# Kernel tuning notes

Measured on AMD Instinct MI355X. Metric: run time of the kernel, lower is better.

The kernel has to match this reference:

```python
import jax, jax.numpy as jnp
import numpy as np

B, S, H = 4, 1024, 2048
E = 16            # num_experts
K = 2             # num_experts_per_token
I = 1024          # per-expert intermediate_dim
N_SHARED = 2
I_SHARED = I * N_SHARED
RATIO = 0.1       # shared_expert_ratio
EPS = 1e-9


def _swiglu(x, wg, wu, wd):
    # SwiGLU, bias=False: down( silu(gate(x)) * up(x) )
    return (jax.nn.silu(x @ wg) * (x @ wu)) @ wd


def setup_inputs() -> dict:
    key = jax.random.key(0)
    ks = jax.random.split(key, 9)
    scale = 0.02
    x = jax.random.normal(ks[0], (B, S, H), dtype=jnp.float32)
    centroids = jax.random.normal(ks[1], (E, H), dtype=jnp.float32)  # nn.Parameter(randn)
    gate_bias = jnp.zeros((E,), dtype=jnp.float32)
    # shared expert SwiGLU weights (intermediate = I * n_shared_experts)
    wg_s = jax.random.normal(ks[2], (H, I_SHARED), dtype=jnp.float32) * scale
    wu_s = jax.random.normal(ks[3], (H, I_SHARED), dtype=jnp.float32) * scale
    wd_s = jax.random.normal(ks[4], (I_SHARED, H), dtype=jnp.float32) * scale
    # routed experts, stacked [E, ...]
    wg = jax.random.normal(ks[5], (E, H, I), dtype=jnp.float32) * scale
    wu = jax.random.normal(ks[6], (E, H, I), dtype=jnp.float32) * scale
    wd = jax.random.normal(ks[7], (E, I, H), dtype=jnp.float32) * scale
    return {"x": x, "centroids": centroids, "gate_bias": gate_bias,
            "wg_s": wg_s, "wu_s": wu_s, "wd_s": wd_s,
            "wg": wg, "wu": wu, "wd": wd}


def reference(x, centroids, gate_bias, wg_s, wu_s, wd_s, wg, wu, wd):
    # 1) shared expert on ALL tokens, scaled by ratio
    shared = _swiglu(x, wg_s, wu_s, wd_s) * RATIO          # [B,S,H]
    # 2) centroid affinity (DeepSeek-V3 sigmoid gating)
    affinity = jax.nn.sigmoid(jnp.einsum('bsh,eh->bse', x, centroids))  # [B,S,E]
    # 3) bias used ONLY for selection
    biased = affinity + gate_bias
    _, top_idx = jax.lax.top_k(biased, K)                  # [B,S,K]
    # 4) clean weights from unbiased affinity, normalized to sum 1
    top_aff = jnp.take_along_axis(affinity, top_idx, axis=-1)  # [B,S,K]
    weights = top_aff / (top_aff.sum(-1, keepdims=True) + EPS)
    # 5) combine-mask: per-token per-expert weight (0 if not selected)
    mask = (jax.nn.one_hot(top_idx, E, dtype=x.dtype) * weights[..., None]).sum(-2)  # [B,S,E]
    # 6) expert compute + weighted combine; loop over fixed small E avoids
    #    materializing a [B,S,E,H] tensor
    routed = jnp.zeros_like(x)
    for e in range(E):
        routed = routed + mask[..., e:e + 1] * _swiglu(x, wg[e], wu[e], wd[e])
    return shared + routed
```

## Files before the change

kernel.cpp:

```cpp
#include <hip/hip_runtime.h>
#include <hip/hip_bf16.h>

typedef unsigned short u16;
typedef unsigned int u32;
typedef unsigned long long u64;
typedef __attribute__((ext_vector_type(8))) short short8;
typedef __attribute__((ext_vector_type(4))) float f32x4;

#define TOKENS 4096
#define HDIM 2048
#define NEXP 16
#define IDIM 1024
#define ISH 2048
#define NCHUNK 128

#define GUITEMS 2304
#define GUCHUNK 288
#define DITEMS 2048
#define DCHUNK 256

#define AS1(p) ((const __attribute__((address_space(1))) u32*)(p))
#define AS3(p) ((__attribute__((address_space(3))) u32*)(p))

__device__ __forceinline__ u16 f2b(float f) {
    u32 u = __float_as_uint(f);
    u32 r = u + 0x7fffu + ((u >> 16) & 1u);
    return (u16)(r >> 16);
}

__global__ __launch_bounds__(256) void convert_x_kernel(const float* __restrict__ x,
                                                        u16* __restrict__ xb) {
    size_t i = ((size_t)blockIdx.x * 256 + threadIdx.x) * 8;
    float4 a = *(const float4*)(x + i);
    float4 b = *(const float4*)(x + i + 4);
    u32 p0 = (u32)f2b(a.x) | ((u32)f2b(a.y) << 16);
    u32 p1 = (u32)f2b(a.z) | ((u32)f2b(a.w) << 16);
    u32 p2 = (u32)f2b(b.x) | ((u32)f2b(b.y) << 16);
    u32 p3 = (u32)f2b(b.z) | ((u32)f2b(b.w) << 16);
    uint4 o = make_uint4(p0, p1, p2, p3);
    *(uint4*)(xb + i) = o;
}

__global__ __launch_bounds__(256) void route_kernel(const float* __restrict__ x,
                                                    const float* __restrict__ cent,
                                                    const float* __restrict__ bias,
                                                    int* __restrict__ top_e,
                                                    float* __restrict__ top_w) {
    __shared__ alignas(16) float cs[8 * 2048];
    int lane = threadIdx.x & 63;
    int wv = threadIdx.x >> 6;
    int t = blockIdx.x * 4 + wv;
    const float4* xp4 = (const float4*)(x + (size_t)t * HDIM);
    float4 xr[8];
#pragma unroll
    for (int i = 0; i < 8; i++) xr[i] = xp4[lane + 64 * i];
    float aff[16];
#pragma unroll
    for (int ph = 0; ph < 2; ph++) {
        if (ph) __syncthreads();
        const float* sbase = cent + (size_t)(ph * 8 + wv * 2) * HDIM;
        float* dbase = cs + (size_t)wv * 2 * HDIM;
#pragma unroll
        for (int i = 0; i < 16; i++) {
            __builtin_amdgcn_global_load_lds(AS1(sbase + i * 256 + lane * 4),
                                             AS3(dbase + i * 256), 16, 0, 0);
        }
        __syncthreads();
#pragma unroll
        for (int e = 0; e < 8; e++) {
            const float4* cp = (const float4*)cs + (size_t)e * 512;
            float s = 0.f;
#pragma unroll
            for (int i = 0; i < 8; i++) {
                float4 cv = cp[lane + 64 * i];
                s += xr[i].x * cv.x;
                s += xr[i].y * cv.y;
                s += xr[i].z * cv.z;
                s += xr[i].w * cv.w;
            }
#pragma unroll
            for (int off = 32; off > 0; off >>= 1) s += __shfl_xor(s, off, 64);
            aff[ph * 8 + e] = 1.f / (1.f + expf(-s));
        }
    }
    float b0 = -1e30f, b1 = -1e30f, a0 = 0.f, a1 = 0.f;
    int e0 = -1, e1 = -1;
#pragma unroll
    for (int e = 0; e < 16; e++) {
        float v = aff[e] + bias[e];
        if (v > b0) {
            b1 = b0; e1 = e0; a1 = a0;
            b0 = v; e0 = e; a0 = aff[e];
        } else if (v > b1) {
            b1 = v; e1 = e; a1 = aff[e];
        }
    }
    float inv = 1.f / (a0 + a1 + 1e-9f);
    if (lane == 0) {
        top_e[2 * t] = e0; top_w[2 * t] = a0 * inv;
        top_e[2 * t + 1] = e1; top_w[2 * t + 1] = a1 * inv;
    }
}

__global__ __launch_bounds__(1024) void build_kernel(
    const int* __restrict__ top_e, const float* __restrict__ top_w,
    int* __restrict__ counts, int* __restrict__ offsets, int* __restrict__ itemsGU,
    int* __restrict__ itemsD, int* __restrict__ list_tok, int* __restrict__ tok2slot) {
    __shared__ int cnt[NCHUNK][16];
    __shared__ int offs_s[16];
    __shared__ int totals[16];
    __shared__ int guPref[16], dPref[16];
    int tid = threadIdx.x;
    int lane = tid & 63, wv = tid >> 6;
    for (int i = tid; i < GUITEMS; i += 1024) itemsGU[i] = -1;
    for (int i = tid; i < DITEMS; i += 1024) itemsD[i] = -1;
    for (int c = wv; c < NCHUNK; c += 16) {
        int v = top_e[c * 64 + lane];
#pragma unroll
        for (int e = 0; e < 16; e++) {
            u64 m = __ballot(v == e);
            if (lane == 0) cnt[c][e] = (int)__popcll(m);
        }
    }
    __syncthreads();
    if (tid < 16) {
        int s = 0;
        for (int c = 0; c < NCHUNK; c++) s += cnt[c][tid];
        totals[tid] = s;
        counts[tid] = s;
    }
    __syncthreads();
    if (tid == 0) {
        int r = 0, g = 0, d = 0;
        for (int e = 0; e < 16; e++) {
            offs_s[e] = r;
            offsets[e] = r;
            r += totals[e];
            guPref[e] = g;
            g += ((totals[e] + 127) >> 7) * 16;
            dPref[e] = d;
            d += ((totals[e] + 255) >> 8) * 32;
        }
    }
    {
        int i = tid;
        int g = i >> 4, s = i & 15;
        int y0 = (g >> 3) << 2, m0 = (g & 7) << 2;
        itemsGU[i] = ((m0 + (s >> 2)) << 8) | (y0 + (s & 3));
    }
    if (tid < 512) {
        int i = tid;
        int g = i >> 4, s = i & 15;
        int y0 = (g >> 2) << 2, m0 = (g & 3) << 2;
        itemsD[i] = ((m0 + (s >> 2)) << 8) | (y0 + (s & 3));
    }
    __syncthreads();
    if (tid < 16) {
        int e = tid;
        int tA = (totals[e] + 127) >> 7;
        int p = 1024 + guPref[e];
        for (int y0 = 0; y0 < 16; y0 += 4)
            for (int m = 0; m < tA; m++)
                for (int dy = 0; dy < 4; dy++)
                    itemsGU[p++] = (1 << 28) | (e << 20) | (m << 8) | (y0 + dy);
        int tB = (totals[e] + 255) >> 8;
        p = 512 + dPref[e];
        for (int y0 = 0; y0 < 32; y0 += 4)
            for (int m = 0; m < tB; m++)
                for (int dy = 0; dy < 4; dy++)
                    itemsD[p++] = (1 << 28) | (e << 20) | (m << 8) | (y0 + dy);
        int r = offs_s[e];
        for (int c = 0; c < NCHUNK; c++) {
            int v = cnt[c][e];
            cnt[c][e] = r;
            r += v;
        }
    }
    __syncthreads();
    for (int c = wv; c < NCHUNK; c += 16) {
        int i = c * 64 + lane;
        int v = top_e[i];
        int rank = 0;
#pragma unroll
        for (int e = 0; e < 16; e++) {
            u64 m = __ballot(v == e);
            if (v == e) rank = (int)__popcll(m & ((1ull << lane) - 1ull));
        }
        int slot = cnt[c][v] + rank;
        list_tok[slot] = i >> 1;
        tok2slot[i] = slot;
    }
}

__global__ __launch_bounds__(256) void conv_w_kernel(const float* __restrict__ W,
                                                     const float* __restrict__ W2,
                                                     u16* __restrict__ Wt,
                                                     u16* __restrict__ Wt2, int K, int N,
                                                     int zsplit) {
    int nt = blockIdx.x, kc = blockIdx.y;
    int zz = blockIdx.z;
    const float* Wm;
    u16* Wtm;
    if (zz < zsplit) {
        Wm = W + (size_t)zz * K * N;
        Wtm = Wt + (size_t)zz * K * N;
    } else {
        int z2 = zz - zsplit;
        Wm = W2 + (size_t)z2 * K * N;
        Wtm = Wt2 + (size_t)z2 * K * N;
    }
    int ksB = K >> 5;
    __shared__ u16 Ls[64 * 40];
    int t = threadIdx.x;
    int kr = t >> 3, ng = t & 7;
    int nn = t >> 2, seg = t & 3;
    int g = seg ^ ((nn >> 2) & 3);
#pragma unroll
    for (int s = 0; s < 8; s++) {
        int kb = kc * 256 + s * 32;
        const float* src = Wm + (size_t)(kb + kr) * N + nt * 64 + ng * 8;
        float4 f0 = *(const float4*)src;
        float4 f1 = *(const float4*)(src + 4);
        __syncthreads();
        const float* p0 = (const float*)&f0;
        const float* p1 = (const float*)&f1;
#pragma unroll
        for (int l = 0; l < 4; l++) Ls[(8 * ng + l) * 40 + kr] = f2b(p0[l]);
#pragma unroll
        for (int l = 0; l < 4; l++) Ls[(8 * ng + 4 + l) * 40 + kr] = f2b(p1[l]);
        __syncthreads();
        const u16* lp = &Ls[nn * 40 + g * 8];
        u32 w0 = (u32)lp[0] | ((u32)lp[1] << 16);
        u32 w1 = (u32)lp[2] | ((u32)lp[3] << 16);
        u32 w2 = (u32)lp[4] | ((u32)lp[5] << 16);
        u32 w3 = (u32)lp[6] | ((u32)lp[7] << 16);
        uint4 o = make_uint4(w0, w1, w2, w3);
        *(uint4*)(Wtm + (size_t)(nt * ksB + (kb >> 5)) * 2048 + t * 8) = o;
    }
}

__global__ __launch_bounds__(256) void gemm_gateup(
    const u16* __restrict__ A, const u16* __restrict__ BgS, const u16* __restrict__ BuS,
    const u16* __restrict__ BgR, const u16* __restrict__ BuR, u16* __restrict__ hS,
    u16* __restrict__ hR, const int* __restrict__ counts, const int* __restrict__ offsets,
    const int* __restrict__ list_tok, const int* __restrict__ items) {
    int idx = (blockIdx.x & 7) * GUCHUNK + (blockIdx.x >> 3);
    int it = items[idx];
    if (it < 0) return;
    int routed = (it >> 28) & 1;
    int e = (it >> 20) & 15;
    int m0 = ((it >> 8) & 4095) * 128;
    int yb = it & 255;
    int cnt, base, Nout;
    const u16 *Bg, *Bu;
    u16* hout;
    if (routed) {
        cnt = counts[e];
        base = offsets[e];
        Nout = IDIM;
        size_t off = (size_t)e * HDIM * IDIM;
        Bg = BgR + off;
        Bu = BuR + off;
        hout = hR;
    } else {
        cnt = TOKENS;
        base = 0;
        Nout = ISH;
        Bg = BgS;
        Bu = BuS;
        hout = hS;
    }
    const int nk = HDIM >> 6;
    __shared__ alignas(16) u16 As[128 * 64];
    __shared__ alignas(16) u16 Bgs[64 * 64];
    __shared__ alignas(16) u16 Bus[64 * 64];
    int tid = threadIdx.x;
    int lane = tid & 63, wv = tid >> 6;
    int quad = lane >> 4, mr = lane & 15;
    int n0 = yb * 64;
    int gk = (tid & 3) ^ ((tid >> 4) & 3);
    int mg0 = min(m0 + (tid >> 2), cnt - 1);
    int mg1 = min(m0 + 64 + (tid >> 2), cnt - 1);
    size_t sr0 = routed ? (size_t)list_tok[base + mg0] : (size_t)mg0;
    size_t sr1 = routed ? (size_t)list_tok[base + mg1] : (size_t)mg1;
    const u16* ap0 = A + sr0 * HDIM + gk * 8;
    const u16* ap1 = A + sr1 * HDIM + gk * 8;
    size_t bstr = (size_t)(HDIM >> 5) * 2048;
    const u16* bgp = Bg + (size_t)yb * bstr + tid * 8;
    const u16* bup = Bu + (size_t)yb * bstr + tid * 8;
    int xq = quad ^ ((mr >> 2) & 3);
    f32x4 accg[2][4], accu[2][4];
#pragma unroll
    for (int i = 0; i < 2; i++)
#pragma unroll
        for (int j = 0; j < 4; j++) { accg[i][j] = (f32x4)0.f; accu[i][j] = (f32x4)0.f; }

    for (int ks = 0; ks < nk; ks++) {
        __syncthreads();
        __builtin_amdgcn_global_load_lds(AS1(ap0), AS3(As + wv * 512), 16, 0, 0);
        __builtin_amdgcn_global_load_lds(AS1(ap0 + 32), AS3(As + 4096 + wv * 512), 16, 0, 0);
        __builtin_amdgcn_global_load_lds(AS1(ap1), AS3(As + 2048 + wv * 512), 16, 0, 0);
        __builtin_amdgcn_global_load_lds(AS1(ap1 + 32), AS3(As + 6144 + wv * 512), 16, 0, 0);
        __builtin_amdgcn_global_load_lds(AS1(bgp), AS3(Bgs + wv * 512), 16, 0, 0);
        __builtin_amdgcn_global_load_lds(AS1(bgp + 2048), AS3(Bgs + 2048 + wv * 512), 16, 0, 0);
        __builtin_amdgcn_global_load_lds(AS1(bup), AS3(Bus + wv * 512), 16, 0, 0);
        __builtin_amdgcn_global_load_lds(AS1(bup + 2048), AS3(Bus + 2048 + wv * 512), 16, 0, 0);
        ap0 += 64; ap1 += 64; bgp += 4096; bup += 4096;
        __syncthreads();
#pragma unroll
        for (int c = 0; c < 2; c++) {
            short8 a0 = *(const short8*)(As + c * 4096 + ((32 * wv + mr) * 4 + xq) * 8);
            short8 a1 = *(const short8*)(As + c * 4096 + ((32 * wv + 16 + mr) * 4 + xq) * 8);
#pragma unroll
            for (int j = 0; j < 4; j++) {
                short8 bg = *(const short8*)(Bgs + c * 2048 + (64 * j + mr * 4 + xq) * 8);
                short8 bu = *(const short8*)(Bus + c * 2048 + (64 * j + mr * 4 + xq) * 8);
                accg[0][j] = __builtin_amdgcn_mfma_f32_16x16x32_bf16(a0, bg, accg[0][j], 0, 0, 0);
                accg[1][j] = __builtin_amdgcn_mfma_f32_16x16x32_bf16(a1, bg, accg[1][j], 0, 0, 0);
                accu[0][j] = __builtin_amdgcn_mfma_f32_16x16x32_bf16(a0, bu, accu[0][j], 0, 0, 0);
                accu[1][j] = __builtin_amdgcn_mfma_f32_16x16x32_bf16(a1, bu, accu[1][j], 0, 0, 0);
            }
        }
    }
#pragma unroll
    for (int i = 0; i < 2; i++)
#pragma unroll
        for (int j = 0; j < 4; j++)
#pragma unroll
            for (int r = 0; r < 4; r++) {
                int m = m0 + 32 * wv + 16 * i + quad * 4 + r;
                if (m < cnt) {
                    float gv = accg[i][j][r], uv = accu[i][j][r];
                    float h = gv / (1.f + expf(-gv)) * uv;
                    int n = n0 + 16 * j + mr;
                    hout[(size_t)(base + m) * Nout + n] = f2b(h);
                }
            }
}

__global__ __launch_bounds__(256) void gemm_down(
    const u16* __restrict__ hS, const u16* __restrict__ hR, const u16* __restrict__ BdS,
    const u16* __restrict__ BdR, float* __restrict__ out, float* __restrict__ rd,
    const int* __restrict__ counts, const int* __restrict__ offsets,
    const int* __restrict__ items) {
    int idx = (blockIdx.x & 7) * DCHUNK + (blockIdx.x >> 3);
    int it = items[idx];
    if (it < 0) return;
    int routed = (it >> 28) & 1;
    int e = (it >> 20) & 15;
    int m0 = ((it >> 8) & 4095) * 256;
    int yb = it & 255;
    int cnt, base, Kd;
    const u16 *A, *B;
    float* outp;
    if (routed) {
        cnt = counts[e];
        base = offsets[e];
        Kd = IDIM;
        A = hR;
        B = BdR + (size_t)e * IDIM * HDIM;
        outp = rd;
    } else {
        cnt = TOKENS;
        base = 0;
        Kd = ISH;
        A = hS;
        B = BdS;
        outp = out;
    }
    int nk = Kd >> 6;
    __shared__ alignas(16) u16 As[256 * 64];
    __shared__ alignas(16) u16 Bs[64 * 64];
    int tid = threadIdx.x;
    int lane = tid & 63, wv = tid >> 6;
    int quad = lane >> 4, mr = lane & 15;
    int n0 = yb * 64;
    int gk = (tid & 3) ^ ((tid >> 4) & 3);
    const u16* ap0;
    const u16* ap1;
    const u16* ap2;
    const u16* ap3;
    {
        int mg0 = base + min(m0 + 0 * 64 + (tid >> 2), cnt - 1);
        int mg1 = base + min(m0 + 1 * 64 + (tid >> 2), cnt - 1);
        int mg2 = base + min(m0 + 2 * 64 + (tid >> 2), cnt - 1);
        int mg3 = base + min(m0 + 3 * 64 + (tid >> 2), cnt - 1);
        ap0 = A + (size_t)mg0 * Kd + gk * 8;
        ap1 = A + (size_t)mg1 * Kd + gk * 8;
        ap2 = A + (size_t)mg2 * Kd + gk * 8;
        ap3 = A + (size_t)mg3 * Kd + gk * 8;
    }
    size_t bstr = (size_t)(Kd >> 5) * 2048;
    const u16* bp = B + (size_t)yb * bstr + tid * 8;
    int xq = quad ^ ((mr >> 2) & 3);
    f32x4 acc[4][4];
#pragma unroll
    for (int i = 0; i < 4; i++)
#pragma unroll
        for (int j = 0; j < 4; j++) acc[i][j] = (f32x4)0.f;

    for (int ks = 0; ks < nk; ks++) {
        __syncthreads();
        __builtin_amdgcn_global_load_lds(AS1(ap0), AS3(As + 0 + wv * 512), 16, 0, 0);
        __builtin_amdgcn_global_load_lds(AS1(ap0 + 32), AS3(As + 8192 + wv * 512), 16, 0, 0);
        __builtin_amdgcn_global_load_lds(AS1(ap1), AS3(As + 2048 + wv * 512), 16, 0, 0);
        __builtin_amdgcn_global_load_lds(AS1(ap1 + 32), AS3(As + 10240 + wv * 512), 16, 0, 0);
        __builtin_amdgcn_global_load_lds(AS1(ap2), AS3(As + 4096 + wv * 512), 16, 0, 0);
        __builtin_amdgcn_global_load_lds(AS1(ap2 + 32), AS3(As + 12288 + wv * 512), 16, 0, 0);
        __builtin_amdgcn_global_load_lds(AS1(ap3), AS3(As + 6144 + wv * 512), 16, 0, 0);
        __builtin_amdgcn_global_load_lds(AS1(ap3 + 32), AS3(As + 14336 + wv * 512), 16, 0, 0);
        __builtin_amdgcn_global_load_lds(AS1(bp), AS3(Bs + wv * 512), 16, 0, 0);
        __builtin_amdgcn_global_load_lds(AS1(bp + 2048), AS3(Bs + 2048 + wv * 512), 16, 0, 0);
        ap0 += 64; ap1 += 64; ap2 += 64; ap3 += 64; bp += 4096;
        __syncthreads();
#pragma unroll
        for (int c = 0; c < 2; c++) {
            short8 a0 = *(const short8*)(As + c * 8192 + ((64 * wv + 0 + mr) * 4 + xq) * 8);
            short8 a1 = *(const short8*)(As + c * 8192 + ((64 * wv + 16 + mr) * 4 + xq) * 8);
            short8 a2 = *(const short8*)(As + c * 8192 + ((64 * wv + 32 + mr) * 4 + xq) * 8);
            short8 a3 = *(const short8*)(As + c * 8192 + ((64 * wv + 48 + mr) * 4 + xq) * 8);
#pragma unroll
            for (int j = 0; j < 4; j++) {
                short8 b = *(const short8*)(Bs + c * 2048 + (64 * j + mr * 4 + xq) * 8);
                acc[0][j] = __builtin_amdgcn_mfma_f32_16x16x32_bf16(a0, b, acc[0][j], 0, 0, 0);
                acc[1][j] = __builtin_amdgcn_mfma_f32_16x16x32_bf16(a1, b, acc[1][j], 0, 0, 0);
                acc[2][j] = __builtin_amdgcn_mfma_f32_16x16x32_bf16(a2, b, acc[2][j], 0, 0, 0);
                acc[3][j] = __builtin_amdgcn_mfma_f32_16x16x32_bf16(a3, b, acc[3][j], 0, 0, 0);
            }
        }
    }

#pragma unroll
    for (int i = 0; i < 4; i++)
#pragma unroll
        for (int j = 0; j < 4; j++)
#pragma unroll
            for (int r = 0; r < 4; r++) {
                int m = m0 + 64 * wv + 16 * i + quad * 4 + r;
                if (m >= cnt) continue;
                int n = n0 + 16 * j + mr;
                float v = acc[i][j][r];
                if (routed) {
                    outp[(size_t)(base + m) * HDIM + n] = v;
                } else {
                    outp[(size_t)m * HDIM + n] = 0.1f * v;
                }
            }
}

__global__ __launch_bounds__(256) void combine_kernel(float* __restrict__ out,
                                                      const float* __restrict__ rd,
                                                      const int* __restrict__ tok2slot,
                                                      const float* __restrict__ top_w) {
    int t = blockIdx.x;
    int s0 = tok2slot[2 * t], s1 = tok2slot[2 * t + 1];
    float w0 = top_w[2 * t], w1 = top_w[2 * t + 1];
    const float4* r0 = (const float4*)(rd + (size_t)s0 * HDIM);
    const float4* r1 = (const float4*)(rd + (size_t)s1 * HDIM);
    float4* op = (float4*)(out + (size_t)t * HDIM);
#pragma unroll
    for (int k = 0; k < 2; k++) {
        int c = threadIdx.x + k * 256;
        float4 o = op[c];
        float4 a = r0[c];
        float4 b = r1[c];
        o.x += w0 * a.x + w1 * b.x;
        o.y += w0 * a.y + w1 * b.y;
        o.z += w0 * a.z + w1 * b.z;
        o.w += w0 * a.w + w1 * b.w;
        op[c] = o;
    }
}

extern "C" void kernel_launch(void* const* d_in, const int* in_sizes, int n_in,
                              void* d_out, int out_size, void* d_ws, size_t ws_size,
                              hipStream_t stream) {
    const float* x = (const float*)d_in[0];
    const float* cent = (const float*)d_in[1];
    const float* bias = (const float*)d_in[2];
    const float* wgs = (const float*)d_in[3];
    const float* wus = (const float*)d_in[4];
    const float* wds = (const float*)d_in[5];
    const float* wg = (const float*)d_in[6];
    const float* wu = (const float*)d_in[7];
    const float* wd = (const float*)d_in[8];
    float* out = (float*)d_out;
    char* ws = (char*)d_ws;

    size_t off_wtgs = 0;
    size_t off_wtus = off_wtgs + (size_t)HDIM * ISH * 2;
    size_t off_wtds = off_wtus + (size_t)HDIM * ISH * 2;
    size_t off_wtg = off_wtds + (size_t)ISH * HDIM * 2;
    size_t off_wtu = off_wtg + (size_t)NEXP * HDIM * IDIM * 2;
    size_t off_wtd = off_wtu + (size_t)NEXP * HDIM * IDIM * 2;
    size_t off_xbf = off_wtd + (size_t)NEXP * IDIM * HDIM * 2;
    size_t off_hsh = off_xbf + (size_t)TOKENS * HDIM * 2;
    size_t off_hrt = off_hsh + (size_t)TOKENS * ISH * 2;
    size_t off_meta = off_hrt + (size_t)2 * TOKENS * IDIM * 2;
    size_t need = off_meta + (1 << 20);
    if (ws_size < need) return;

    u16* Wt_gs = (u16*)(ws + off_wtgs);
    u16* Wt_us = (u16*)(ws + off_wtus);
    u16* Wt_ds = (u16*)(ws + off_wtds);
    u16* Wt_g = (u16*)(ws + off_wtg);
    u16* Wt_u = (u16*)(ws + off_wtu);
    u16* Wt_d = (u16*)(ws + off_wtd);
    u16* x_bf = (u16*)(ws + off_xbf);
    u16* h_sh = (u16*)(ws + off_hsh);
    u16* h_rt = (u16*)(ws + off_hrt);
    float* rd = (float*)(ws + off_wtg);
    int* counts = (int*)(ws + off_meta);
    int* offsets = counts + 16;
    int* itemsGU = offsets + 16;
    int* itemsD = itemsGU + GUITEMS;
    int* tok2slot = itemsD + DITEMS;
    int* top_e = tok2slot + 2 * TOKENS;
    float* top_w = (float*)(top_e + 2 * TOKENS);
    int* list_tok = (int*)(top_w + 2 * TOKENS);

    convert_x_kernel<<<TOKENS * HDIM / (256 * 8), 256, 0, stream>>>(x, x_bf);
    route_kernel<<<TOKENS / 4, 256, 0, stream>>>(x, cent, bias, top_e, top_w);
    build_kernel<<<1, 1024, 0, stream>>>(top_e, top_w, counts, offsets, itemsGU, itemsD,
                                         list_tok, tok2slot);

    conv_w_kernel<<<dim3(ISH / 64, HDIM / 256, 2), 256, 0, stream>>>(
        wgs, wus, Wt_gs, Wt_us, HDIM, ISH, 1);
    conv_w_kernel<<<dim3(HDIM / 64, ISH / 256, 1), 256, 0, stream>>>(
        wds, wds, Wt_ds, Wt_ds, ISH, HDIM, 1);
    conv_w_kernel<<<dim3(IDIM / 64, HDIM / 256, 2 * NEXP), 256, 0, stream>>>(
        wg, wu, Wt_g, Wt_u, HDIM, IDIM, NEXP);
    conv_w_kernel<<<dim3(HDIM / 64, IDIM / 256, NEXP), 256, 0, stream>>>(
        wd, wd, Wt_d, Wt_d, IDIM, HDIM, NEXP);

    gemm_gateup<<<GUITEMS, 256, 0, stream>>>(x_bf, Wt_gs, Wt_us, Wt_g, Wt_u, h_sh, h_rt,
                                             counts, offsets, list_tok, itemsGU);
    gemm_down<<<DITEMS, 256, 0, stream>>>(h_sh, h_rt, Wt_ds, Wt_d, out, rd, counts,
                                          offsets, itemsD);
    combine_kernel<<<TOKENS, 256, 0, stream>>>(out, rd, tok2slot, top_w);
}
```

Measured before the change: 927.6 us.

## Fuse x conversion into routing, merge weight conversions, remap item indices

The fp32-to-bf16 conversion of x now happens inside the routing kernel, reusing the x registers it already loads, so the separate convert kernel and its extra read of x go away. The four weight-conversion launches become a single flat-grid kernel that decodes which matrix and tile to handle from the block id. The block-to-item mapping in both GEMMs changes from chunked striding to a new interleaved formula, which alters the order items are scheduled across XCDs. The new mapping has to match the item list the build kernel produces, or work items may be skipped or computed twice.

```diff
diff --git a/kernel.cpp b/kernel.cpp
--- a/kernel.cpp
+++ b/kernel.cpp
@@ -15,9 +15,7 @@
 #define NCHUNK 128
 
 #define GUITEMS 2304
-#define GUCHUNK 288
 #define DITEMS 2048
-#define DCHUNK 256
 
 #define AS1(p) ((const __attribute__((address_space(1))) u32*)(p))
 #define AS3(p) ((__attribute__((address_space(3))) u32*)(p))
@@ -28,22 +26,15 @@
     return (u16)(r >> 16);
 }
 
-__global__ __launch_bounds__(256) void convert_x_kernel(const float* __restrict__ x,
-                                                        u16* __restrict__ xb) {
-    size_t i = ((size_t)blockIdx.x * 256 + threadIdx.x) * 8;
-    float4 a = *(const float4*)(x + i);
-    float4 b = *(const float4*)(x + i + 4);
-    u32 p0 = (u32)f2b(a.x) | ((u32)f2b(a.y) << 16);
-    u32 p1 = (u32)f2b(a.z) | ((u32)f2b(a.w) << 16);
-    u32 p2 = (u32)f2b(b.x) | ((u32)f2b(b.y) << 16);
-    u32 p3 = (u32)f2b(b.z) | ((u32)f2b(b.w) << 16);
-    uint4 o = make_uint4(p0, p1, p2, p3);
-    *(uint4*)(xb + i) = o;
+__device__ __forceinline__ int item_index(int bid) {
+    int x = bid & 7, j = bid >> 3;
+    return ((x + 8 * (j >> 4)) << 4) | (j & 15);
 }
 
 __global__ __launch_bounds__(256) void route_kernel(const float* __restrict__ x,
                                                     const float* __restrict__ cent,
                                                     const float* __restrict__ bias,
+                                                    u16* __restrict__ xb,
                                                     int* __restrict__ top_e,
                                                     float* __restrict__ top_w) {
     __shared__ alignas(16) float cs[8 * 2048];
@@ -54,6 +45,14 @@
     float4 xr[8];
 #pragma unroll
     for (int i = 0; i < 8; i++) xr[i] = xp4[lane + 64 * i];
+    u16* xbp = xb + (size_t)t * HDIM;
+#pragma unroll
+    for (int i = 0; i < 8; i++) {
+        u32 lo = (u32)f2b(xr[i].x) | ((u32)f2b(xr[i].y) << 16);
+        u32 hi = (u32)f2b(xr[i].z) | ((u32)f2b(xr[i].w) << 16);
+        uint2 o = make_uint2(lo, hi);
+        *(uint2*)(xbp + (size_t)(lane + 64 * i) * 4) = o;
+    }
     float aff[16];
 #pragma unroll
     for (int ph = 0; ph < 2; ph++) {
@@ -192,29 +191,49 @@
     }
 }
 
-__global__ __launch_bounds__(256) void conv_w_kernel(const float* __restrict__ W,
-                                                     const float* __restrict__ W2,
-                                                     u16* __restrict__ Wt,
-                                                     u16* __restrict__ Wt2, int K, int N,
-                                                     int zsplit) {
-    int nt = blockIdx.x, kc = blockIdx.y;
-    int zz = blockIdx.z;
+__global__ __launch_bounds__(256) void conv_all_kernel(
+    const float* __restrict__ wgs, const float* __restrict__ wus,
+    const float* __restrict__ wds, const float* __restrict__ wg,
+    const float* __restrict__ wu, const float* __restrict__ wd, u16* __restrict__ Wt_gs,
+    u16* __restrict__ Wt_us, u16* __restrict__ Wt_ds, u16* __restrict__ Wt_g,
+    u16* __restrict__ Wt_u, u16* __restrict__ Wt_d) {
+    int id = blockIdx.x;
     const float* Wm;
     u16* Wtm;
-    if (zz < zsplit) {
-        Wm = W + (size_t)zz * K * N;
-        Wtm = Wt + (size_t)zz * K * N;
+    int K, N, nt, kc;
+    if (id < 768) {
+        K = 2048; N = 2048;
+        int seg = id >> 8, r = id & 255;
+        nt = r & 31; kc = r >> 5;
+        if (seg == 0) { Wm = wgs; Wtm = Wt_gs; }
+        else if (seg == 1) { Wm = wus; Wtm = Wt_us; }
+        else { Wm = wds; Wtm = Wt_ds; }
+    } else if (id < 4864) {
+        K = 2048; N = 1024;
+        int r = id - 768;
+        int m = r >> 11;
+        r &= 2047;
+        int e = r >> 7;
+        r &= 127;
+        nt = r & 15; kc = r >> 4;
+        size_t off = (size_t)e * 2048 * 1024;
+        if (m == 0) { Wm = wg + off; Wtm = Wt_g + off; }
+        else { Wm = wu + off; Wtm = Wt_u + off; }
     } else {
-        int z2 = zz - zsplit;
-        Wm = W2 + (size_t)z2 * K * N;
-        Wtm = Wt2 + (size_t)z2 * K * N;
+        K = 1024; N = 2048;
+        int r = id - 4864;
+        int e = r >> 7;
+        r &= 127;
+        nt = r & 31; kc = r >> 5;
+        size_t off = (size_t)e * 1024 * 2048;
+        Wm = wd + off; Wtm = Wt_d + off;
     }
     int ksB = K >> 5;
     __shared__ u16 Ls[64 * 40];
     int t = threadIdx.x;
     int kr = t >> 3, ng = t & 7;
-    int nn = t >> 2, seg = t & 3;
-    int g = seg ^ ((nn >> 2) & 3);
+    int nn = t >> 2, seg2 = t & 3;
+    int g = seg2 ^ ((nn >> 2) & 3);
 #pragma unroll
     for (int s = 0; s < 8; s++) {
         int kb = kc * 256 + s * 32;
@@ -244,8 +263,7 @@
     const u16* __restrict__ BgR, const u16* __restrict__ BuR, u16* __restrict__ hS,
     u16* __restrict__ hR, const int* __restrict__ counts, const int* __restrict__ offsets,
     const int* __restrict__ list_tok, const int* __restrict__ items) {
-    int idx = (blockIdx.x & 7) * GUCHUNK + (blockIdx.x >> 3);
-    int it = items[idx];
+    int it = items[item_index(blockIdx.x)];
     if (it < 0) return;
     int routed = (it >> 28) & 1;
     int e = (it >> 20) & 15;
@@ -343,8 +361,7 @@
     const u16* __restrict__ BdR, float* __restrict__ out, float* __restrict__ rd,
     const int* __restrict__ counts, const int* __restrict__ offsets,
     const int* __restrict__ items) {
-    int idx = (blockIdx.x & 7) * DCHUNK + (blockIdx.x >> 3);
-    int it = items[idx];
+    int it = items[item_index(blockIdx.x)];
     if (it < 0) return;
     int routed = (it >> 28) & 1;
     int e = (it >> 20) & 15;
@@ -519,20 +536,11 @@
     float* top_w = (float*)(top_e + 2 * TOKENS);
     int* list_tok = (int*)(top_w + 2 * TOKENS);
 
-    convert_x_kernel<<<TOKENS * HDIM / (256 * 8), 256, 0, stream>>>(x, x_bf);
-    route_kernel<<<TOKENS / 4, 256, 0, stream>>>(x, cent, bias, top_e, top_w);
+    route_kernel<<<TOKENS / 4, 256, 0, stream>>>(x, cent, bias, x_bf, top_e, top_w);
     build_kernel<<<1, 1024, 0, stream>>>(top_e, top_w, counts, offsets, itemsGU, itemsD,
                                          list_tok, tok2slot);
-
-    conv_w_kernel<<<dim3(ISH / 64, HDIM / 256, 2), 256, 0, stream>>>(
-        wgs, wus, Wt_gs, Wt_us, HDIM, ISH, 1);
-    conv_w_kernel<<<dim3(HDIM / 64, ISH / 256, 1), 256, 0, stream>>>(
-        wds, wds, Wt_ds, Wt_ds, ISH, HDIM, 1);
-    conv_w_kernel<<<dim3(IDIM / 64, HDIM / 256, 2 * NEXP), 256, 0, stream>>>(
-        wg, wu, Wt_g, Wt_u, HDIM, IDIM, NEXP);
-    conv_w_kernel<<<dim3(HDIM / 64, IDIM / 256, NEXP), 256, 0, stream>>>(
-        wd, wd, Wt_d, Wt_d, IDIM, HDIM, NEXP);
-
+    conv_all_kernel<<<6912, 256, 0, stream>>>(wgs, wus, wds, wg, wu, wd, Wt_gs, Wt_us,
+                                              Wt_ds, Wt_g, Wt_u, Wt_d);
     gemm_gateup<<<GUITEMS, 256, 0, stream>>>(x_bf, Wt_gs, Wt_us, Wt_g, Wt_u, h_sh, h_rt,
                                              counts, offsets, list_tok, itemsGU);
     gemm_down<<<DITEMS, 256, 0, stream>>>(h_sh, h_rt, Wt_ds, Wt_d, out, rd, counts,
```

Measured after the change: 865.8 us. 1.07x faster.
